# Kernel tuning notes

Hardware: AMD Instinct MI355X
Metric: run time of the kernel (lower is better)

## Reference

```python
import jax, jax.numpy as jnp
import numpy as np

WIN = 5
EPS = 1e-05


def box_sum(x, win=WIN):
    """3D box-filter window sum, SAME padding (pad=win//2), via separable 1D convs.
    Mathematically identical to F.conv3d(x, ones(1,1,win,win,win), padding=win//2).
    x: [N, C, D, H, W]
    """
    pad = win // 2
    for ax in range(3):  # D, H, W
        kshape = [1, 1, 1, 1, 1]
        kshape[2 + ax] = win
        k = jnp.ones(kshape, x.dtype)
        pads = [(0, 0), (0, 0), (0, 0)]
        pads[ax] = (pad, pad)
        x = jax.lax.conv_general_dilated(
            x, k, window_strides=(1, 1, 1), padding=pads,
            dimension_numbers=('NCDHW', 'OIDHW', 'NCDHW'))
    return x


def setup_inputs() -> dict:
    key = jax.random.key(0)
    k1, k2 = jax.random.split(key)
    shape = (2, 1, 160, 192, 192)
    I = jax.random.normal(k1, shape, dtype=jnp.float32)
    J = jax.random.normal(k2, shape, dtype=jnp.float32)
    return {"I": I, "J": J}


def reference(I, J):
    V = float(WIN ** 3)  # window voxel count
    I_sum = box_sum(I)
    J_sum = box_sum(J)
    I2_sum = box_sum(I * I)
    J2_sum = box_sum(J * J)
    IJ_sum = box_sum(I * J)

    u_I = I_sum / V
    u_J = J_sum / V
    cross = IJ_sum - u_J * I_sum - u_I * J_sum + u_I * u_J * V
    I_var = I2_sum - 2.0 * u_I * I_sum + u_I * u_I * V
    J_var = J2_sum - 2.0 * u_J * J_sum + u_J * u_J * V
    cc = cross * cross / (I_var * J_var + EPS)
    # single channel: avg over channels is identity; loss = -mean(cc)
    return -1.0 * jnp.mean(cc)
```

## Files before the change

### kernel.cpp

```cpp
#include <hip/hip_runtime.h>


namespace {
constexpr int Wd = 192, Hd = 192, Dd = 160;
constexpr int SH = 192;
constexpr int SD = 192 * 192;
constexpr long SN = (long)SD * Dd;
constexpr int CD = 6;
constexpr int NCHUNK = 27;
constexpr int TROW = 68;
constexpr int ROWS = 20;
constexpr int SEGA = 17 * ROWS;
constexpr int TILEF = 2 * ROWS * TROW;
constexpr float INV_V = 1.0f / 125.0f;
constexpr float EPSf = 1e-5f;

__device__ __forceinline__ void wslide(const float h[8], float o[4]) {
  float s0 = h[0] + h[1] + h[2] + h[3] + h[4];
  float s1 = s0 - h[0] + h[5];
  float s2 = s1 - h[1] + h[6];
  float s3 = s2 - h[2] + h[7];
  o[0] = s0; o[1] = s1; o[2] = s2; o[3] = s3;
}

__device__ __forceinline__ void gl_lds16(const float* g, float* l) {
  __builtin_amdgcn_global_load_lds(
      (const __attribute__((address_space(1))) void*)g,
      (__attribute__((address_space(3))) void*)l, 16, 0, 0);
}
}

__global__ __launch_bounds__(256) void ncc_fused(const float* __restrict__ I,
                                                 const float* __restrict__ Jv,
                                                 float* __restrict__ out) {
  __shared__ float tile[2][TILEF];
  __shared__ float red[4];

  const int tid = threadIdx.x;
  const int tx = tid & 15;
  const int ty = tid >> 4;
  const int wbase = blockIdx.x * 64;
  const int hbase = blockIdx.y * 16;
  const int n  = blockIdx.z / NCHUNK;
  const int d_lo = (blockIdx.z % NCHUNK) * CD;

  const float* Ib = I  + (long)n * SN;
  const float* Jb = Jv + (long)n * SN;

  const int wave = tid >> 6, lane = tid & 63;
  const float* gsrc = (wave >= 2) ? Jb : Ib;
  int goff[3]; int loff[3]; bool on[3];
  #pragma unroll
  for (int r = 0; r < 3; ++r) {
    const int seg = wave * 170 + r * 64 + lane;
    on[r] = (r < 2) || (lane < 42);
    const int rem = seg % SEGA;
    const int row = rem / 17, c16 = rem % 17;
    const int hh = hbase + row - 2;
    const int hc = min(max(hh, 0), Hd - 1);
    const int gw = wbase - 2 + c16 * 4;
    const int gc = min(max(gw, 0), Wd - 4);
    goff[r] = hc * SH + gc;
    loff[r] = seg * 4;
  }

  {
    const int s0 = d_lo - 2;
    if (s0 >= 0 && s0 < Dd) {
      const float* base = gsrc + (long)s0 * SD;
      #pragma unroll
      for (int r = 0; r < 3; ++r) if (on[r]) gl_lds16(base + goff[r], &tile[0][loff[r]]);
    }
  }
  __syncthreads();

  const bool zl = (wbase == 0)   && (tx == 0);
  const bool zr = (wbase == 128) && (tx == 15);

  float ring[5][5][4];
  float Dsum[5][4];
  #pragma unroll
  for (int c = 0; c < 5; ++c) {
    #pragma unroll
    for (int k = 0; k < 4; ++k) {
      Dsum[c][k] = 0.f;
      #pragma unroll
      for (int q = 0; q < 5; ++q) ring[q][c][k] = 0.f;
    }
  }
  float acc = 0.0f;

  constexpr int T = CD + 4;
  for (int t0 = 0; t0 < T; t0 += 5) {
    #pragma unroll
    for (int p = 0; p < 5; ++p) {
      const int t = t0 + p;
      const int s = d_lo - 2 + t;

      {
        const int sn = s + 1;
        if ((t + 1) < T && sn >= 0 && sn < Dd) {
          const float* base = gsrc + (long)sn * SD;
          float* dst = &tile[(t + 1) & 1][0];
          #pragma unroll
          for (int r = 0; r < 3; ++r) if (on[r]) gl_lds16(base + goff[r], dst + loff[r]);
        }
      }

      float hsI[8], hsJ[8], hsII[8], hsJJ[8], hsIJ[8];
      #pragma unroll
      for (int c = 0; c < 8; ++c) {
        hsI[c] = 0.f; hsJ[c] = 0.f; hsII[c] = 0.f; hsJJ[c] = 0.f; hsIJ[c] = 0.f;
      }
      if (s >= 0 && s < Dd) {
        const float* bufc = &tile[t & 1][0];
        #pragma unroll
        for (int dh = 0; dh < 5; ++dh) {
          const int rrow = ty + dh;
          const int hh = hbase + rrow - 2;
          if (hh >= 0 && hh < Hd) {
            const float* pa = bufc + rrow * TROW + 4 * tx;
            const float* pb = pa + ROWS * TROW;
            float a[8], b[8];
            ((float4*)a)[0] = ((const float4*)pa)[0];
            ((float4*)a)[1] = ((const float4*)pa)[1];
            ((float4*)b)[0] = ((const float4*)pb)[0];
            ((float4*)b)[1] = ((const float4*)pb)[1];
            if (zl) { a[2]=a[0]; a[3]=a[1]; a[0]=0.f; a[1]=0.f;
                      b[2]=b[0]; b[3]=b[1]; b[0]=0.f; b[1]=0.f; }
            if (zr) { a[4]=a[6]; a[5]=a[7]; a[6]=0.f; a[7]=0.f;
                      b[4]=b[6]; b[5]=b[7]; b[6]=0.f; b[7]=0.f; }
            #pragma unroll
            for (int c = 0; c < 8; ++c) {
              const float x = a[c], y = b[c];
              hsI[c]  += x;
              hsJ[c]  += y;
              hsII[c] = fmaf(x, x, hsII[c]);
              hsJJ[c] = fmaf(y, y, hsJJ[c]);
              hsIJ[c] = fmaf(x, y, hsIJ[c]);
            }
          }
        }
      }

      float nw[5][4];
      wslide(hsI,  nw[0]);
      wslide(hsJ,  nw[1]);
      wslide(hsII, nw[2]);
      wslide(hsJJ, nw[3]);
      wslide(hsIJ, nw[4]);
      #pragma unroll
      for (int c = 0; c < 5; ++c) {
        #pragma unroll
        for (int k = 0; k < 4; ++k) {
          Dsum[c][k] += nw[c][k] - ring[p][c][k];
          ring[p][c][k] = nw[c][k];
        }
      }

      const int d = d_lo + t - 4;
      if (t >= 4 && d < Dd) {
        #pragma unroll
        for (int k = 0; k < 4; ++k) {
          const float SI = Dsum[0][k], SJ = Dsum[1][k];
          const float SII = Dsum[2][k], SJJ = Dsum[3][k], SIJ = Dsum[4][k];
          const float cross = SIJ - SI * SJ * INV_V;
          const float vI    = SII - SI * SI * INV_V;
          const float vJ    = SJJ - SJ * SJ * INV_V;
          acc += cross * cross / (vI * vJ + EPSf);
        }
      }

      __syncthreads();
    }
  }

  #pragma unroll
  for (int off = 32; off > 0; off >>= 1) acc += __shfl_xor(acc, off, 64);
  if ((tid & 63) == 0) red[tid >> 6] = acc;
  __syncthreads();
  if (tid == 0) {
    const float total = red[0] + red[1] + red[2] + red[3];
    atomicAdd(out, total * (-1.0f / 11796480.0f));
  }
}

extern "C" void kernel_launch(void* const* d_in, const int* in_sizes, int n_in,
                              void* d_out, int out_size, void* d_ws, size_t ws_size,
                              hipStream_t stream) {
  const float* I = (const float*)d_in[0];
  const float* J = (const float*)d_in[1];
  float* out = (float*)d_out;
  hipMemsetAsync(out, 0, sizeof(float), stream);
  dim3 grid(3, 12, 2 * NCHUNK);
  ncc_fused<<<grid, 256, 0, stream>>>(I, J, out);
}
```

Before: 167.9 us.

## Use single-wave blocks without barriers, deeper depth chunks, interior fast path

```diff
diff --git a/kernel.cpp b/kernel.cpp
--- a/kernel.cpp
+++ b/kernel.cpp
@@ -6,12 +6,12 @@
 constexpr int SH = 192;
 constexpr int SD = 192 * 192;
 constexpr long SN = (long)SD * Dd;
-constexpr int CD = 6;
-constexpr int NCHUNK = 27;
-constexpr int TROW = 68;
-constexpr int ROWS = 20;
-constexpr int SEGA = 17 * ROWS;
-constexpr int TILEF = 2 * ROWS * TROW;
+constexpr int CD = 16;
+constexpr int NCHUNK = 10;
+constexpr int SEGS = 216;
+constexpr int BUF  = SEGS * 4;
+constexpr int RROW = 36;
+constexpr int AOFF = 12 * RROW;
 constexpr float INV_V = 1.0f / 125.0f;
 constexpr float EPSf = 1e-5f;
 
@@ -30,64 +30,58 @@
 }
 }
 
-__global__ __launch_bounds__(256) void ncc_fused(const float* __restrict__ I,
-                                                 const float* __restrict__ Jv,
-                                                 float* __restrict__ out) {
-  __shared__ float tile[2][TILEF];
-  __shared__ float red[4];
-
-  const int tid = threadIdx.x;
-  const int tx = tid & 15;
-  const int ty = tid >> 4;
-  const int wbase = blockIdx.x * 64;
-  const int hbase = blockIdx.y * 16;
+__global__ __launch_bounds__(64) void ncc_fused(const float* __restrict__ I,
+                                                const float* __restrict__ Jv,
+                                                float* __restrict__ out) {
+  __shared__ float tile[2][BUF];
+
+  const int lane = threadIdx.x;
+  const int tx = lane & 7;
+  const int ty = lane >> 3;
+  const int wbase = blockIdx.x * 32;
+  const int hbase = blockIdx.y * 8;
   const int n  = blockIdx.z / NCHUNK;
   const int d_lo = (blockIdx.z % NCHUNK) * CD;
 
   const float* Ib = I  + (long)n * SN;
   const float* Jb = Jv + (long)n * SN;
 
-  const int wave = tid >> 6, lane = tid & 63;
-  const float* gsrc = (wave >= 2) ? Jb : Ib;
-  int goff[3]; int loff[3]; bool on[3];
+  const float* gbase[4]; int loff[4]; bool on[4];
   #pragma unroll
-  for (int r = 0; r < 3; ++r) {
-    const int seg = wave * 170 + r * 64 + lane;
-    on[r] = (r < 2) || (lane < 42);
-    const int rem = seg % SEGA;
-    const int row = rem / 17, c16 = rem % 17;
+  for (int r = 0; r < 4; ++r) {
+    const int seg = r * 64 + lane;
+    on[r] = (r < 3) || (lane < SEGS - 192);
+    const int a = (seg >= 108) ? 1 : 0;
+    const int rem = seg - a * 108;
+    const int row = rem / 9, c16 = rem % 9;
     const int hh = hbase + row - 2;
     const int hc = min(max(hh, 0), Hd - 1);
-    const int gw = wbase - 2 + c16 * 4;
+    const int gw = wbase - 2 + 4 * c16;
     const int gc = min(max(gw, 0), Wd - 4);
-    goff[r] = hc * SH + gc;
+    gbase[r] = (a ? Jb : Ib) + (hc * SH + gc);
     loff[r] = seg * 4;
   }
 
-  {
-    const int s0 = d_lo - 2;
-    if (s0 >= 0 && s0 < Dd) {
-      const float* base = gsrc + (long)s0 * SD;
-      #pragma unroll
-      for (int r = 0; r < 3; ++r) if (on[r]) gl_lds16(base + goff[r], &tile[0][loff[r]]);
-    }
+  if (d_lo >= 2) {
+    const long off = (long)(d_lo - 2) * SD;
+    #pragma unroll
+    for (int r = 0; r < 4; ++r) if (on[r]) gl_lds16(gbase[r] + off, &tile[0][loff[r]]);
   }
-  __syncthreads();
 
   const bool zl = (wbase == 0)   && (tx == 0);
-  const bool zr = (wbase == 128) && (tx == 15);
+  const bool zr = (wbase == 160) && (tx == 7);
+  const bool hint = (hbase != 0) && (hbase != 184);
 
   float ring[5][5][4];
   float Dsum[5][4];
   #pragma unroll
-  for (int c = 0; c < 5; ++c) {
+  for (int c = 0; c < 5; ++c)
     #pragma unroll
     for (int k = 0; k < 4; ++k) {
       Dsum[c][k] = 0.f;
       #pragma unroll
       for (int q = 0; q < 5; ++q) ring[q][c][k] = 0.f;
     }
-  }
   float acc = 0.0f;
 
   constexpr int T = CD + 4;
@@ -100,39 +94,37 @@
       {
         const int sn = s + 1;
         if ((t + 1) < T && sn >= 0 && sn < Dd) {
-          const float* base = gsrc + (long)sn * SD;
+          const long off = (long)sn * SD;
           float* dst = &tile[(t + 1) & 1][0];
           #pragma unroll
-          for (int r = 0; r < 3; ++r) if (on[r]) gl_lds16(base + goff[r], dst + loff[r]);
+          for (int r = 0; r < 4; ++r) if (on[r]) gl_lds16(gbase[r] + off, dst + loff[r]);
         }
       }
 
       float hsI[8], hsJ[8], hsII[8], hsJJ[8], hsIJ[8];
-      #pragma unroll
-      for (int c = 0; c < 8; ++c) {
-        hsI[c] = 0.f; hsJ[c] = 0.f; hsII[c] = 0.f; hsJJ[c] = 0.f; hsIJ[c] = 0.f;
-      }
-      if (s >= 0 && s < Dd) {
+      const bool svalid = (s >= 0) && (s < Dd);
+      if (svalid && hint) {
         const float* bufc = &tile[t & 1][0];
         #pragma unroll
         for (int dh = 0; dh < 5; ++dh) {
-          const int rrow = ty + dh;
-          const int hh = hbase + rrow - 2;
-          if (hh >= 0 && hh < Hd) {
-            const float* pa = bufc + rrow * TROW + 4 * tx;
-            const float* pb = pa + ROWS * TROW;
-            float a[8], b[8];
-            ((float4*)a)[0] = ((const float4*)pa)[0];
-            ((float4*)a)[1] = ((const float4*)pa)[1];
-            ((float4*)b)[0] = ((const float4*)pb)[0];
-            ((float4*)b)[1] = ((const float4*)pb)[1];
-            if (zl) { a[2]=a[0]; a[3]=a[1]; a[0]=0.f; a[1]=0.f;
-                      b[2]=b[0]; b[3]=b[1]; b[0]=0.f; b[1]=0.f; }
-            if (zr) { a[4]=a[6]; a[5]=a[7]; a[6]=0.f; a[7]=0.f;
-                      b[4]=b[6]; b[5]=b[7]; b[6]=0.f; b[7]=0.f; }
-            #pragma unroll
-            for (int c = 0; c < 8; ++c) {
-              const float x = a[c], y = b[c];
+          const float* pa = bufc + (ty + dh) * RROW + 4 * tx;
+          const float* pb = pa + AOFF;
+          float a[8], b[8];
+          ((float4*)a)[0] = ((const float4*)pa)[0];
+          ((float4*)a)[1] = ((const float4*)pa)[1];
+          ((float4*)b)[0] = ((const float4*)pb)[0];
+          ((float4*)b)[1] = ((const float4*)pb)[1];
+          if (zl) { a[2]=a[0]; a[3]=a[1]; a[0]=0.f; a[1]=0.f;
+                    b[2]=b[0]; b[3]=b[1]; b[0]=0.f; b[1]=0.f; }
+          if (zr) { a[4]=a[6]; a[5]=a[7]; a[6]=0.f; a[7]=0.f;
+                    b[4]=b[6]; b[5]=b[7]; b[6]=0.f; b[7]=0.f; }
+          #pragma unroll
+          for (int c = 0; c < 8; ++c) {
+            const float x = a[c], y = b[c];
+            if (dh == 0) {
+              hsI[c] = x; hsJ[c] = y;
+              hsII[c] = x * x; hsJJ[c] = y * y; hsIJ[c] = x * y;
+            } else {
               hsI[c]  += x;
               hsJ[c]  += y;
               hsII[c] = fmaf(x, x, hsII[c]);
@@ -141,6 +133,40 @@
             }
           }
         }
+      } else {
+        #pragma unroll
+        for (int c = 0; c < 8; ++c) {
+          hsI[c] = 0.f; hsJ[c] = 0.f; hsII[c] = 0.f; hsJJ[c] = 0.f; hsIJ[c] = 0.f;
+        }
+        if (svalid) {
+          const float* bufc = &tile[t & 1][0];
+          #pragma unroll
+          for (int dh = 0; dh < 5; ++dh) {
+            const int hh = hbase + ty + dh - 2;
+            if (hh >= 0 && hh < Hd) {
+              const float* pa = bufc + (ty + dh) * RROW + 4 * tx;
+              const float* pb = pa + AOFF;
+              float a[8], b[8];
+              ((float4*)a)[0] = ((const float4*)pa)[0];
+              ((float4*)a)[1] = ((const float4*)pa)[1];
+              ((float4*)b)[0] = ((const float4*)pb)[0];
+              ((float4*)b)[1] = ((const float4*)pb)[1];
+              if (zl) { a[2]=a[0]; a[3]=a[1]; a[0]=0.f; a[1]=0.f;
+                        b[2]=b[0]; b[3]=b[1]; b[0]=0.f; b[1]=0.f; }
+              if (zr) { a[4]=a[6]; a[5]=a[7]; a[6]=0.f; a[7]=0.f;
+                        b[4]=b[6]; b[5]=b[7]; b[6]=0.f; b[7]=0.f; }
+              #pragma unroll
+              for (int c = 0; c < 8; ++c) {
+                const float x = a[c], y = b[c];
+                hsI[c]  += x;
+                hsJ[c]  += y;
+                hsII[c] = fmaf(x, x, hsII[c]);
+                hsJJ[c] = fmaf(y, y, hsJJ[c]);
+                hsIJ[c] = fmaf(x, y, hsIJ[c]);
+              }
+            }
+          }
+        }
       }
 
       float nw[5][4];
@@ -150,16 +176,14 @@
       wslide(hsJJ, nw[3]);
       wslide(hsIJ, nw[4]);
       #pragma unroll
-      for (int c = 0; c < 5; ++c) {
+      for (int c = 0; c < 5; ++c)
         #pragma unroll
         for (int k = 0; k < 4; ++k) {
           Dsum[c][k] += nw[c][k] - ring[p][c][k];
           ring[p][c][k] = nw[c][k];
         }
-      }
-
-      const int d = d_lo + t - 4;
-      if (t >= 4 && d < Dd) {
+
+      if (t >= 4) {
         #pragma unroll
         for (int k = 0; k < 4; ++k) {
           const float SI = Dsum[0][k], SJ = Dsum[1][k];
@@ -170,19 +194,12 @@
           acc += cross * cross / (vI * vJ + EPSf);
         }
       }
-
-      __syncthreads();
     }
   }
 
   #pragma unroll
   for (int off = 32; off > 0; off >>= 1) acc += __shfl_xor(acc, off, 64);
-  if ((tid & 63) == 0) red[tid >> 6] = acc;
-  __syncthreads();
-  if (tid == 0) {
-    const float total = red[0] + red[1] + red[2] + red[3];
-    atomicAdd(out, total * (-1.0f / 11796480.0f));
-  }
+  if (lane == 0) atomicAdd(out, acc * (-1.0f / 11796480.0f));
 }
 
 extern "C" void kernel_launch(void* const* d_in, const int* in_sizes, int n_in,
@@ -192,6 +209,6 @@
   const float* J = (const float*)d_in[1];
   float* out = (float*)d_out;
   hipMemsetAsync(out, 0, sizeof(float), stream);
-  dim3 grid(3, 12, 2 * NCHUNK);
-  ncc_fused<<<grid, 256, 0, stream>>>(I, J, out);
-}
+  dim3 grid(6, 24, 2 * NCHUNK);
+  ncc_fused<<<grid, 64, 0, stream>>>(I, J, out);
+}
```

After: 186.3 us. +11.0%, slower.
